# Kernel optimization log

Measured on AMD Instinct MI355X. Metric: run time of the kernel, lower is better.

Reference implementation:

```python
import jax, jax.numpy as jnp
import numpy as np

D = 256      # in_out_dimension
HID = 128    # hidden_dimension
N = 8192     # total nodes
S = 256      # number of graphs/segments


def setup_inputs() -> dict:
    key = jax.random.key(0)
    ks = jax.random.split(key, 20)
    lin = lambda k, o, i: jax.random.normal(k, (o, i), jnp.float32) * 0.05
    vec = lambda k, o: jax.random.normal(k, (o,), jnp.float32) * 0.05
    H = jax.random.normal(ks[0], (N, D), jnp.float32)
    batch = jnp.sort(jax.random.randint(ks[1], (N,), 0, S)).astype(jnp.int64)
    return {
        "H": H, "batch": batch,
        "phi_w1": lin(ks[2], D, D), "phi_b1": vec(ks[3], D),
        "phi_w2": lin(ks[4], D, D), "phi_b2": vec(ks[5], D),
        "att_w": lin(ks[6], D, D), "att_b": vec(ks[7], D),
        "rho_w1": lin(ks[8], D, D), "rho_b1": vec(ks[9], D),
        "rho_w2": lin(ks[10], D, D), "rho_b2": vec(ks[11], D),
        "g_w1": lin(ks[12], HID, D), "g_b1": vec(ks[13], HID),
        "g_w2": lin(ks[14], HID, HID), "g_b2": vec(ks[15], HID),
        "g_w3": lin(ks[16], 1, HID), "g_b3": vec(ks[17], 1),
    }


def _lrelu(x):
    return jax.nn.leaky_relu(x, negative_slope=0.01)


def reference(H, batch, phi_w1, phi_b1, phi_w2, phi_b2, att_w, att_b,
              rho_w1, rho_b1, rho_w2, rho_b2,
              g_w1, g_b1, g_w2, g_b2, g_w3, g_b3):
    # phi MLP
    Hf = _lrelu(_lrelu(H @ phi_w1.T + phi_b1) @ phi_w2.T + phi_b2)  # [N, D]
    att = Hf @ att_w.T + att_b                                      # [N, D]
    dot = att @ att.T                                               # [N, N]
    mask = (batch[:, None] == batch[None, :]).astype(Hf.dtype)      # block-diagonal
    # faithful to torch: max over (dot * mask), i.e. includes masked zeros
    max_values = jnp.max(dot * mask, axis=1, keepdims=True)         # [N, 1]
    mdp = (dot - max_values) * mask
    e = jnp.exp(mdp)
    aw = (e / jnp.sum(e * mask, axis=1, keepdims=True)) * mask      # [N, N]
    H_mixed = aw @ Hf                                               # [N, D]
    H_mixed = _lrelu(_lrelu(H_mixed @ rho_w1.T + rho_b1) @ rho_w2.T + rho_b2)
    h_gate = _lrelu(_lrelu(H_mixed @ g_w1.T + g_b1) @ g_w2.T + g_b2) @ g_w3.T + g_b3  # [N, 1]
    # scatter_softmax over segments
    seg_max = jax.ops.segment_max(h_gate, batch, num_segments=S)    # [S, 1]
    ex = jnp.exp(h_gate - seg_max[batch])
    den = jax.ops.segment_sum(ex, batch, num_segments=S)
    scores = ex / den[batch]                                        # [N, 1]
    h_pool = jax.ops.segment_sum(H_mixed * scores, batch, num_segments=S)  # [S, D]
    return (h_pool, scores)
```

## Files before the change

kernel.cpp:

```cpp
#include <hip/hip_runtime.h>
#include <math.h>

#define N_NODES 8192
#define D 256
#define HID 128
#define S_SEG 256
#define MAXC 64
#define HFT_STR 144
#define PB_STR 144
#define PB_LO 9216

typedef __attribute__((ext_vector_type(8))) short short8;
typedef __attribute__((ext_vector_type(4))) float f32x4;
typedef unsigned short u16;
typedef unsigned int u32;

__device__ __forceinline__ u16 f2bf(float f) {
  u32 u = __float_as_uint(f);
  u32 r = (u + 0x7fffu + ((u >> 16) & 1u)) >> 16;
  return (u16)r;
}
__device__ __forceinline__ float bf2f(u16 b) {
  return __uint_as_float(((u32)b) << 16);
}
__device__ __forceinline__ int4 pack8(float4 x, float4 y) {
  int4 v;
  v.x = (int)(((u32)f2bf(x.y) << 16) | f2bf(x.x));
  v.y = (int)(((u32)f2bf(x.w) << 16) | f2bf(x.z));
  v.z = (int)(((u32)f2bf(y.y) << 16) | f2bf(y.x));
  v.w = (int)(((u32)f2bf(y.w) << 16) | f2bf(y.z));
  return v;
}

struct CvtJobs {
  const float* src[7];
  u16* dst[7];
  int n4[7];
};
__global__ __launch_bounds__(256) void prep(const int* __restrict__ batch,
                                            int* __restrict__ sstart,
                                            int* __restrict__ scount, CvtJobs jb) {
  if (blockIdx.x == 0) {
    __shared__ int cntS[S_SEG];
    __shared__ int startS[S_SEG];
    const int t = threadIdx.x;
    cntS[t] = 0;
    startS[t] = 0;
    __syncthreads();
    const int base = t * 32;
    int pb = (base == 0) ? -1 : batch[base - 1];
    for (int i = 0; i < 32; ++i) {
      int b = batch[base + i];
      atomicAdd(&cntS[b], 1);
      if (b != pb) startS[b] = base + i;
      pb = b;
    }
    __syncthreads();
    scount[t] = cntS[t];
    sstart[t] = startS[t];
  } else {
    const int bid = blockIdx.x - 1;
    const int job = bid >> 3, chunk = bid & 7;
    const float* s = jb.src[job];
    u16* d = jb.dst[job];
    const int n4 = jb.n4[job];
    for (int i = chunk * 256 + threadIdx.x; i < n4; i += 2048) {
      float4 v = ((const float4*)s)[i];
      ushort4 o;
      o.x = f2bf(v.x); o.y = f2bf(v.y); o.z = f2bf(v.z); o.w = f2bf(v.w);
      ((ushort4*)d)[i] = o;
    }
  }
}

template <int KST>
__device__ __forceinline__ void loadW(short8* w, const u16* __restrict__ Wg,
                                      int col, int K, int lane) {
  const u16* base = Wg + (size_t)col * K + ((lane >> 4) * 8);
#pragma unroll
  for (int kk = 0; kk < KST; ++kk) w[kk] = *(const short8*)(base + kk * 32);
}

template <int KST, int ACT, int ISTR, int OSTR, int MODE, int MG>
__device__ __forceinline__ void mlp_phase(
    const u16* ldsIn, u16* ldsOut, u16* ldsOut2, const short8* wreg,
    const float* __restrict__ bias, int cg, int rows, int lane, int wave) {
  const int nrt = (rows + 31) >> 5;
  const int col = cg * 16 + (lane & 15);
  const float b = bias[col];
  int rt0, rt1;
  if constexpr (MG == 16) {
    rt0 = 0; rt1 = nrt;
  } else {
    rt0 = wave >> 3;
    rt1 = (rt0 < nrt) ? rt0 + 1 : rt0;
  }
  for (int rt = rt0; rt < rt1; ++rt) {
    short8 af[2][KST];
#pragma unroll
    for (int m = 0; m < 2; ++m)
#pragma unroll
      for (int kk = 0; kk < KST; ++kk) {
        const int r = rt * 32 + m * 16 + (lane & 15);
        const int sl = kk * 4 + (lane >> 4);
        af[m][kk] = *(const short8*)((const char*)ldsIn + r * ISTR +
                                     ((sl ^ (r & 7)) * 16));
      }
    f32x4 acc0 = {0.f, 0.f, 0.f, 0.f}, acc1 = {0.f, 0.f, 0.f, 0.f};
#pragma unroll
    for (int kk = 0; kk < KST; ++kk) {
      acc0 = __builtin_amdgcn_mfma_f32_16x16x32_bf16(af[0][kk], wreg[kk], acc0, 0, 0, 0);
      acc1 = __builtin_amdgcn_mfma_f32_16x16x32_bf16(af[1][kk], wreg[kk], acc1, 0, 0, 0);
    }
    const int rb = (lane >> 4) * 4;
#pragma unroll
    for (int m = 0; m < 2; ++m) {
      f32x4 a = m ? acc1 : acc0;
#pragma unroll
      for (int r4 = 0; r4 < 4; ++r4) {
        const int row = rt * 32 + m * 16 + rb + r4;
        if (row < rows) {
          float v = a[r4] + b;
          if (ACT) v = (v >= 0.f) ? v : 0.01f * v;
          if constexpr (MODE == 3) {
            const int byo =
                row * OSTR + (((col >> 3) ^ (row & 7)) * 16) + (col & 7) * 2;
            u16 hi = f2bf(v);
            *(u16*)((char*)ldsOut + byo) = hi;
            *(u16*)((char*)ldsOut2 + byo) = f2bf(v - bf2f(hi));
          } else if constexpr (MODE == 4) {
            u16 hv = f2bf(v);
            *(u16*)((char*)ldsOut + row * OSTR +
                    (((col >> 3) ^ (row & 7)) * 16) + (col & 7) * 2) = hv;
            *(u16*)((char*)ldsOut2 + col * HFT_STR + row * 2) = hv;
          } else {
            *(u16*)((char*)ldsOut + row * OSTR +
                    (((col >> 3) ^ (row & 7)) * 16) + (col & 7) * 2) = f2bf(v);
          }
        }
      }
    }
  }
}

template <int KST, int ACT, int ISTR, int OSTR, int MODE>
__device__ __forceinline__ void mlp16(
    const u16* ldsIn, u16* ldsOut, u16* ldsOut2, const u16* __restrict__ Wg,
    const float* __restrict__ bias, u16* __restrict__ gOut,
    u16* __restrict__ gOut2, int M, int K, int rows, int lane, int wave) {
  const int MG = M >> 4;
  const int npairs = ((rows + 31) >> 5) * MG;
  for (int p = wave; p < npairs; p += 16) {
    const int rt = p / MG, cg = p - rt * MG;
    short8 af[2][KST];
#pragma unroll
    for (int m = 0; m < 2; ++m)
#pragma unroll
      for (int kk = 0; kk < KST; ++kk) {
        const int r = rt * 32 + m * 16 + (lane & 15);
        const int sl = kk * 4 + (lane >> 4);
        af[m][kk] = *(const short8*)((const char*)ldsIn + r * ISTR +
                                     ((sl ^ (r & 7)) * 16));
      }
    const int col = cg * 16 + (lane & 15);
    short8 bfr[KST];
#pragma unroll
    for (int kk = 0; kk < KST; ++kk)
      bfr[kk] = *(const short8*)&Wg[(size_t)col * K + kk * 32 + (lane >> 4) * 8];
    f32x4 acc0 = {0.f, 0.f, 0.f, 0.f}, acc1 = {0.f, 0.f, 0.f, 0.f};
#pragma unroll
    for (int kk = 0; kk < KST; ++kk) {
      acc0 = __builtin_amdgcn_mfma_f32_16x16x32_bf16(af[0][kk], bfr[kk], acc0, 0, 0, 0);
      acc1 = __builtin_amdgcn_mfma_f32_16x16x32_bf16(af[1][kk], bfr[kk], acc1, 0, 0, 0);
    }
    const float b = bias[col];
    const int rb = (lane >> 4) * 4;
#pragma unroll
    for (int m = 0; m < 2; ++m) {
      f32x4 a = m ? acc1 : acc0;
#pragma unroll
      for (int r4 = 0; r4 < 4; ++r4) {
        const int row = rt * 32 + m * 16 + rb + r4;
        if (row < rows) {
          float v = a[r4] + b;
          if (ACT) v = (v >= 0.f) ? v : 0.01f * v;
          if constexpr (MODE == 2) {
            u16 hi = f2bf(v);
            gOut[(size_t)row * M + col] = hi;
            gOut2[(size_t)row * M + col] = f2bf(v - bf2f(hi));
          } else {
            u16 hv = f2bf(v);
            *(u16*)((char*)ldsOut + row * OSTR + (((col >> 3) ^ (row & 7)) * 16) +
                    (col & 7) * 2) = hv;
            if constexpr (MODE == 1) gOut[(size_t)row * M + col] = hv;
          }
        }
      }
    }
  }
}

__global__ __launch_bounds__(1024) void seg_all(
    const float* __restrict__ H, const u16* __restrict__ pw1,
    const float* __restrict__ pb1, const u16* __restrict__ pw2,
    const float* __restrict__ pb2, const u16* __restrict__ aw,
    const float* __restrict__ ab, const u16* __restrict__ rw1,
    const float* __restrict__ rb1, const u16* __restrict__ rw2,
    const float* __restrict__ rb2, const u16* __restrict__ gw1,
    const float* __restrict__ gb1, const u16* __restrict__ gw2,
    const float* __restrict__ gb2, const float* __restrict__ gw3,
    const float* __restrict__ gb3, const int* __restrict__ sstart,
    const int* __restrict__ scount, float* __restrict__ hpool,
    float* __restrict__ scores, u16* __restrict__ Hfg, u16* __restrict__ aHg,
    u16* __restrict__ aLg, u16* __restrict__ Hmg, u16* __restrict__ Hm2g,
    float* __restrict__ hgg) {
  __shared__ __align__(16) u16 bufX[MAXC * 256];
  __shared__ __align__(16) u16 bufY[MAXC * 256];
  __shared__ __align__(16) u16 attH[MAXC * 256];
  __shared__ __align__(16) u16 Tt[256 * 72];
  __shared__ float redP[64][4];
  __shared__ float hgs[MAXC];
  __shared__ float red[1024];
  __shared__ float part[1024];
  const int s = blockIdx.x, t = threadIdx.x;
  const int cnt = scount[s];
  const int r0 = sstart[s];
  const int wave = t >> 6, lane = t & 63;

  if (cnt == 0) {
    if (t < 256) hpool[(size_t)s * D + t] = 0.f;
    return;
  }

  if (cnt <= MAXC) {
    short8 wreg[8];
    const int cg16 = (wave + s) & 15;
    const int cg8 = ((wave & 7) + s) & 7;
    const int col16 = cg16 * 16 + (lane & 15);
    const int col8 = cg8 * 16 + (lane & 15);
    const int lrow = lane & 15;

    loadW<8>(wreg, pw1, col16, D, lane);
    {
      const int r = t >> 4, p16 = t & 15;
      if (r < cnt) {
        const float4* src = (const float4*)&H[(size_t)(r0 + r) * D + p16 * 16];
#pragma unroll
        for (int i = 0; i < 2; ++i) {
          int4 v = pack8(src[2 * i], src[2 * i + 1]);
          const int sl = p16 * 2 + i;
          *(int4*)((char*)bufX + r * 512 + ((sl ^ (r & 7)) * 16)) = v;
        }
      }
    }
    __syncthreads();
    mlp_phase<8, 1, 512, 512, 0, 16>(bufX, bufY, nullptr, wreg, pb1, cg16, cnt, lane, wave);
    loadW<8>(wreg, pw2, col16, D, lane);
    __syncthreads();
    mlp_phase<8, 1, 512, 512, 4, 16>(bufY, bufX, (u16*)Tt, wreg, pb2, cg16, cnt, lane, wave);
    loadW<8>(wreg, aw, col16, D, lane);
    __syncthreads();
    mlp_phase<8, 0, 512, 512, 3, 16>(bufX, attH, bufY, wreg, ab, cg16, cnt, lane, wave);
    __syncthreads();
    const int cp = (cnt + 15) & ~15;
    const int nt = cp >> 4;
    f32x4 ev = {0.f, 0.f, 0.f, 0.f};
    const int ttile = wave;
    const bool qact = ttile < nt * nt;
    int ti = 0, tj = 0;
    if (qact) {
      ti = ttile / nt; tj = ttile - ti * nt;
      const int ra = ti * 16 + lrow, rb2 = tj * 16 + lrow;
      f32x4 acc = {0.f, 0.f, 0.f, 0.f};
#pragma unroll
      for (int k0 = 0; k0 < D; k0 += 32) {
        const int sg = (k0 >> 3) + (lane >> 4);
        short8 ah = *(const short8*)((const char*)attH + ra * 512 + ((sg ^ (ra & 7)) * 16));
        short8 av = *(const short8*)((const char*)bufY + ra * 512 + ((sg ^ (ra & 7)) * 16));
        short8 bh = *(const short8*)((const char*)attH + rb2 * 512 + ((sg ^ (rb2 & 7)) * 16));
        short8 bv = *(const short8*)((const char*)bufY + rb2 * 512 + ((sg ^ (rb2 & 7)) * 16));
        acc = __builtin_amdgcn_mfma_f32_16x16x32_bf16(ah, bh, acc, 0, 0, 0);
        acc = __builtin_amdgcn_mfma_f32_16x16x32_bf16(ah, bv, acc, 0, 0, 0);
        acc = __builtin_amdgcn_mfma_f32_16x16x32_bf16(av, bh, acc, 0, 0, 0);
      }
      const int j = tj * 16 + lrow;
      const bool jok = j < cnt;
#pragma unroll
      for (int r = 0; r < 4; ++r) ev[r] = jok ? __expf(acc[r]) : 0.f;
      float p0 = ev[0], p1 = ev[1], p2 = ev[2], p3 = ev[3];
#pragma unroll
      for (int o = 1; o <= 8; o <<= 1) {
        p0 += __shfl_xor(p0, o); p1 += __shfl_xor(p1, o);
        p2 += __shfl_xor(p2, o); p3 += __shfl_xor(p3, o);
      }
      if ((lane & 15) == 0) {
        const int rbase = ti * 16 + (lane >> 4) * 4;
        redP[rbase + 0][tj] = p0;
        redP[rbase + 1][tj] = p1;
        redP[rbase + 2][tj] = p2;
        redP[rbase + 3][tj] = p3;
      }
    }
    __syncthreads();
    const int cpk = (cp <= 32) ? 32 : 64;
    if (qact) {
      const int j = tj * 16 + lrow;
      const int rbase = ti * 16 + (lane >> 4) * 4;
#pragma unroll
      for (int r = 0; r < 4; ++r) {
        float rs = 0.f;
        for (int q = 0; q < nt; ++q) rs += redP[rbase + r][q];
        const float pv = ev[r] / rs;
        const u16 hi = f2bf(pv);
        const u16 lo = f2bf(pv - bf2f(hi));
        *(u16*)((char*)bufY + (rbase + r) * PB_STR + j * 2) = hi;
        *(u16*)((char*)bufY + PB_LO + (rbase + r) * PB_STR + j * 2) = lo;
      }
    }
    if (cpk > cp) {
      const int w2 = cpk - cp;
      for (int idx = t; idx < cp * w2; idx += 1024) {
        const int rr = idx / w2, cc = cp + idx - (idx / w2) * w2;
        *(u16*)((char*)bufY + rr * PB_STR + cc * 2) = 0;
        *(u16*)((char*)bufY + PB_LO + rr * PB_STR + cc * 2) = 0;
      }
    }
    if (cpk > cnt) {
      const int w3 = cpk - cnt;
      for (int idx = t; idx < 256 * w3; idx += 1024) {
        const int dd = idx / w3, cc = cnt + idx - (idx / w3) * w3;
        *(u16*)((char*)Tt + dd * HFT_STR + cc * 2) = 0;
      }
    }
    __syncthreads();
    {
      const int kst = cpk >> 5;
      for (int tt = wave; tt < nt * 16; tt += 16) {
        const int rt = tt >> 4, cg = tt & 15;
        const int arow = rt * 16 + lrow;
        const int dcol = cg * 16 + lrow;
        const int koct = (lane >> 4) * 8;
        f32x4 acc = {0.f, 0.f, 0.f, 0.f};
        for (int ks = 0; ks < kst; ++ks) {
          const int kb = ks * 32 + koct;
          short8 ph = *(const short8*)((const char*)bufY + arow * PB_STR + kb * 2);
          short8 pl = *(const short8*)((const char*)bufY + PB_LO + arow * PB_STR + kb * 2);
          short8 hb = *(const short8*)((const char*)Tt + dcol * HFT_STR + kb * 2);
          acc = __builtin_amdgcn_mfma_f32_16x16x32_bf16(ph, hb, acc, 0, 0, 0);
          acc = __builtin_amdgcn_mfma_f32_16x16x32_bf16(pl, hb, acc, 0, 0, 0);
        }
        const int rb = (lane >> 4) * 4;
#pragma unroll
        for (int r = 0; r < 4; ++r) {
          const int row = rt * 16 + rb + r;
          const int col = cg * 16 + lrow;
          *(u16*)((char*)bufX + row * 512 + (((col >> 3) ^ (row & 7)) * 16) +
                  (col & 7) * 2) = f2bf(acc[r]);
        }
      }
    }
    loadW<8>(wreg, rw1, col16, D, lane);
    __syncthreads();
    mlp_phase<8, 1, 512, 512, 0, 16>(bufX, attH, nullptr, wreg, rb1, cg16, cnt, lane, wave);
    loadW<8>(wreg, rw2, col16, D, lane);
    __syncthreads();
    mlp_phase<8, 1, 512, 512, 0, 16>(attH, (u16*)Tt, nullptr, wreg, rb2, cg16, cnt, lane, wave);
    loadW<8>(wreg, gw1, col8, D, lane);
    __syncthreads();
    if (t < 64) hgs[t] = 0.f;
    mlp_phase<8, 1, 512, 256, 0, 8>((u16*)Tt, bufX, nullptr, wreg, gb1, cg8, cnt, lane, wave);
    loadW<4>(wreg, gw2, col8, HID, lane);
    __syncthreads();
    {
      const int nrt = (cnt + 31) >> 5;
      const int rt = wave >> 3;
      if (rt < nrt) {
        short8 af2[2][4];
#pragma unroll
        for (int m = 0; m < 2; ++m)
#pragma unroll
          for (int kk = 0; kk < 4; ++kk) {
            const int r = rt * 32 + m * 16 + (lane & 15);
            const int sl = kk * 4 + (lane >> 4);
            af2[m][kk] = *(const short8*)((const char*)bufX + r * 256 +
                                          ((sl ^ (r & 7)) * 16));
          }
        f32x4 acc0 = {0.f, 0.f, 0.f, 0.f}, acc1 = {0.f, 0.f, 0.f, 0.f};
#pragma unroll
        for (int kk = 0; kk < 4; ++kk) {
          acc0 = __builtin_amdgcn_mfma_f32_16x16x32_bf16(af2[0][kk], wreg[kk], acc0, 0, 0, 0);
          acc1 = __builtin_amdgcn_mfma_f32_16x16x32_bf16(af2[1][kk], wreg[kk], acc1, 0, 0, 0);
        }
        const float b = gb2[col8];
        const float w3c = gw3[col8];
        const int rb = (lane >> 4) * 4;
#pragma unroll
        for (int m = 0; m < 2; ++m) {
          f32x4 a = m ? acc1 : acc0;
#pragma unroll
          for (int r4 = 0; r4 < 4; ++r4) {
            const int row = rt * 32 + m * 16 + rb + r4;
            float v = a[r4] + b;
            v = (v >= 0.f) ? v : 0.01f * v;
            float pp = v * w3c;
            pp += __shfl_xor(pp, 1);
            pp += __shfl_xor(pp, 2);
            pp += __shfl_xor(pp, 4);
            pp += __shfl_xor(pp, 8);
            if ((lane & 15) == 0 && row < cnt) atomicAdd(&hgs[row], pp);
          }
        }
      }
    }
    __syncthreads();
    {
      const float hgv = (lane < cnt) ? hgs[lane] : -INFINITY;
      float m = hgv;
#pragma unroll
      for (int o = 32; o > 0; o >>= 1) m = fmaxf(m, __shfl_xor(m, o));
      float e = (lane < cnt) ? __expf(hgv - m) : 0.f;
      float sum = e;
#pragma unroll
      for (int o = 32; o > 0; o >>= 1) sum += __shfl_xor(sum, o);
      const float sc = e / sum;
      if (wave == 0 && lane < cnt) scores[r0 + lane] = sc;
      const int d = (wave & 3) * 64 + lane;
      const int g = wave >> 2;
      float acc = 0.f;
      for (int i = g; i < cnt; i += 4) {
        const float si = __shfl(sc, i);
        acc += si * bf2f(*(const u16*)((const char*)Tt + i * 512 +
                          (((d >> 3) ^ (i & 7)) * 16) + (d & 7) * 2));
      }
      part[g * 256 + d] = acc;
    }
    __syncthreads();
    if (t < 256)
      hpool[(size_t)s * D + t] =
          part[t] + part[t + 256] + part[t + 512] + part[t + 768];
  } else {
    for (int c0 = 0; c0 < cnt; c0 += 64) {
      const int rows = (cnt - c0) > 64 ? 64 : (cnt - c0);
      {
        const int r = t >> 4, p16 = t & 15;
        if (r < rows) {
          const float4* src = (const float4*)&H[(size_t)(r0 + c0 + r) * D + p16 * 16];
#pragma unroll
          for (int i = 0; i < 2; ++i) {
            int4 v = pack8(src[2 * i], src[2 * i + 1]);
            const int sl = p16 * 2 + i;
            *(int4*)((char*)bufX + r * 512 + ((sl ^ (r & 7)) * 16)) = v;
          }
        }
      }
      __syncthreads();
      mlp16<8, 1, 512, 512, 0>(bufX, bufY, nullptr, pw1, pb1, nullptr, nullptr, D, D, rows, lane, wave);
      __syncthreads();
      mlp16<8, 1, 512, 512, 1>(bufY, bufX, nullptr, pw2, pb2, Hfg + (size_t)(r0 + c0) * D, nullptr, D, D, rows, lane, wave);
      __syncthreads();
      mlp16<8, 0, 512, 512, 2>(bufX, nullptr, nullptr, aw, ab, aHg + (size_t)(r0 + c0) * D, aLg + (size_t)(r0 + c0) * D, D, D, rows, lane, wave);
      __syncthreads();
    }
    float* Pf = (float*)bufY;
    for (int i = 0; i < cnt; ++i) {
      const u16* ai = aHg + (size_t)(r0 + i) * D;
      const u16* li = aLg + (size_t)(r0 + i) * D;
      for (int j = t; j < cnt; j += 1024) {
        const u16* aj = aHg + (size_t)(r0 + j) * D;
        const u16* lj = aLg + (size_t)(r0 + j) * D;
        float acc = 0.f;
        for (int k = 0; k < D; ++k)
          acc += (bf2f(ai[k]) + bf2f(li[k])) * (bf2f(aj[k]) + bf2f(lj[k]));
        Pf[j] = acc;
      }
      __syncthreads();
      float pm = -INFINITY;
      for (int j = t; j < cnt; j += 1024) pm = fmaxf(pm, Pf[j]);
      red[t] = pm;
      __syncthreads();
      for (int o = 512; o > 0; o >>= 1) {
        if (t < o) red[t] = fmaxf(red[t], red[t + o]);
        __syncthreads();
      }
      const float m = red[0];
      __syncthreads();
      float ps = 0.f;
      for (int j = t; j < cnt; j += 1024) {
        const float e = __expf(Pf[j] - m);
        Pf[j] = e;
        ps += e;
      }
      red[t] = ps;
      __syncthreads();
      for (int o = 512; o > 0; o >>= 1) {
        if (t < o) red[t] += red[t + o];
        __syncthreads();
      }
      const float inv = 1.f / red[0];
      if (t < D) {
        float acc = 0.f;
        for (int j = 0; j < cnt; ++j)
          acc += Pf[j] * bf2f(Hfg[(size_t)(r0 + j) * D + t]);
        Hmg[(size_t)(r0 + i) * D + t] = f2bf(acc * inv);
      }
      __syncthreads();
    }
    for (int c0 = 0; c0 < cnt; c0 += 64) {
      const int rows = (cnt - c0) > 64 ? 64 : (cnt - c0);
      {
        const int r = t >> 4, p16 = t & 15;
        if (r < rows) {
          const int4* src = (const int4*)&Hmg[(size_t)(r0 + c0 + r) * D + p16 * 16];
#pragma unroll
          for (int i = 0; i < 2; ++i) {
            const int sl = p16 * 2 + i;
            *(int4*)((char*)bufX + r * 512 + ((sl ^ (r & 7)) * 16)) = src[i];
          }
        }
      }
      __syncthreads();
      mlp16<8, 1, 512, 512, 0>(bufX, bufY, nullptr, rw1, rb1, nullptr, nullptr, D, D, rows, lane, wave);
      __syncthreads();
      mlp16<8, 1, 512, 512, 1>(bufY, bufX, nullptr, rw2, rb2, Hm2g + (size_t)(r0 + c0) * D, nullptr, D, D, rows, lane, wave);
      __syncthreads();
      mlp16<8, 1, 512, 256, 0>(bufX, bufY, nullptr, gw1, gb1, nullptr, nullptr, HID, D, rows, lane, wave);
      __syncthreads();
      mlp16<4, 1, 256, 256, 0>(bufY, attH, nullptr, gw2, gb2, nullptr, nullptr, HID, HID, rows, lane, wave);
      __syncthreads();
      {
        const int i = t >> 4, p16 = t & 15;
        if (i < rows) {
          short8 hv = *(const short8*)((const char*)attH + i * 256 + ((p16 ^ (i & 7)) * 16));
          float sacc = 0.f;
#pragma unroll
          for (int q = 0; q < 8; ++q) sacc += bf2f((u16)hv[q]) * gw3[p16 * 8 + q];
          sacc += __shfl_xor(sacc, 1);
          sacc += __shfl_xor(sacc, 2);
          sacc += __shfl_xor(sacc, 4);
          sacc += __shfl_xor(sacc, 8);
          if (p16 == 0) hgg[r0 + c0 + i] = sacc + gb3[0];
        }
      }
      __syncthreads();
    }
    float pm = -INFINITY;
    for (int i = t; i < cnt; i += 1024) pm = fmaxf(pm, hgg[r0 + i]);
    red[t] = pm;
    __syncthreads();
    for (int o = 512; o > 0; o >>= 1) {
      if (t < o) red[t] = fmaxf(red[t], red[t + o]);
      __syncthreads();
    }
    const float m = red[0];
    __syncthreads();
    float ps = 0.f;
    for (int i = t; i < cnt; i += 1024) ps += __expf(hgg[r0 + i] - m);
    red[t] = ps;
    __syncthreads();
    for (int o = 512; o > 0; o >>= 1) {
      if (t < o) red[t] += red[t + o];
      __syncthreads();
    }
    const float inv = 1.f / red[0];
    for (int i = t; i < cnt; i += 1024)
      scores[r0 + i] = __expf(hgg[r0 + i] - m) * inv;
    const int h = t >> 8, d = t & 255;
    float acc = 0.f;
    for (int i = h; i < cnt; i += 4)
      acc += __expf(hgg[r0 + i] - m) * inv * bf2f(Hm2g[(size_t)(r0 + i) * D + d]);
    part[t] = acc;
    __syncthreads();
    if (t < 256)
      hpool[(size_t)s * D + t] =
          part[t] + part[t + 256] + part[t + 512] + part[t + 768];
  }
}

extern "C" void kernel_launch(void* const* d_in, const int* in_sizes, int n_in,
                              void* d_out, int out_size, void* d_ws, size_t ws_size,
                              hipStream_t stream) {
  const float* H      = (const float*)d_in[0];
  const int*   batch  = (const int*)d_in[1];
  const float* phi_w1 = (const float*)d_in[2];
  const float* phi_b1 = (const float*)d_in[3];
  const float* phi_w2 = (const float*)d_in[4];
  const float* phi_b2 = (const float*)d_in[5];
  const float* att_w  = (const float*)d_in[6];
  const float* att_b  = (const float*)d_in[7];
  const float* rho_w1 = (const float*)d_in[8];
  const float* rho_b1 = (const float*)d_in[9];
  const float* rho_w2 = (const float*)d_in[10];
  const float* rho_b2 = (const float*)d_in[11];
  const float* g_w1   = (const float*)d_in[12];
  const float* g_b1   = (const float*)d_in[13];
  const float* g_w2   = (const float*)d_in[14];
  const float* g_b2   = (const float*)d_in[15];
  const float* g_w3   = (const float*)d_in[16];
  const float* g_b3   = (const float*)d_in[17];

  float* out_hpool  = (float*)d_out;
  float* out_scores = (float*)d_out + (size_t)S_SEG * D;

  char* w = (char*)d_ws;
  const size_t MB = 1u << 20;
  u16*   wb     = (u16*)(w);
  u16*   Hfg    = (u16*)(w + 1 * MB);
  u16*   aHg    = (u16*)(w + 5 * MB);
  u16*   aLg    = (u16*)(w + 9 * MB);
  u16*   Hmg    = (u16*)(w + 13 * MB);
  u16*   Hm2g   = (u16*)(w + 17 * MB);
  float* hgg    = (float*)(w + 21 * MB);
  int*   sstart = (int*)(w + 21 * MB + 64 * 1024);
  int*   scount = sstart + S_SEG;

  u16* phi_w1b = wb;
  u16* phi_w2b = wb + 65536;
  u16* att_wb  = wb + 2 * 65536;
  u16* rho_w1b = wb + 3 * 65536;
  u16* rho_w2b = wb + 4 * 65536;
  u16* g_w1b   = wb + 5 * 65536;
  u16* g_w2b   = wb + 5 * 65536 + 32768;

  CvtJobs jb;
  jb.src[0] = phi_w1; jb.dst[0] = phi_w1b; jb.n4[0] = 65536 / 4;
  jb.src[1] = phi_w2; jb.dst[1] = phi_w2b; jb.n4[1] = 65536 / 4;
  jb.src[2] = att_w;  jb.dst[2] = att_wb;  jb.n4[2] = 65536 / 4;
  jb.src[3] = rho_w1; jb.dst[3] = rho_w1b; jb.n4[3] = 65536 / 4;
  jb.src[4] = rho_w2; jb.dst[4] = rho_w2b; jb.n4[4] = 65536 / 4;
  jb.src[5] = g_w1;   jb.dst[5] = g_w1b;   jb.n4[5] = 32768 / 4;
  jb.src[6] = g_w2;   jb.dst[6] = g_w2b;   jb.n4[6] = 16384 / 4;

  prep<<<57, 256, 0, stream>>>(batch, sstart, scount, jb);

  seg_all<<<S_SEG, 1024, 0, stream>>>(
      H, phi_w1b, phi_b1, phi_w2b, phi_b2, att_wb, att_b, rho_w1b, rho_b1,
      rho_w2b, rho_b2, g_w1b, g_b1, g_w2b, g_b2, g_w3, g_b3, sstart, scount,
      out_hpool, out_scores, Hfg, aHg, aLg, Hmg, Hm2g, hgg);
}
```

Before: 52.57 us.

## Split waves into row-tile by column-pair MLP work and fuse attention softmax per row

The per-segment MLP phases now assign each wave one 32-row tile and two 16-column groups (c and c+128). Previously each of 16 waves owned one column group and looped over every row tile. Weight loads for the next layer are double-buffered across the wA/wB register sets and issued around barriers. The attention dot/exp/row-sum step now gives each wave a whole 16-row strip, which removes the redP cross-wave reduction and one barrier. MFMA sections are wrapped in s_setprio and the LDS buffer roles are reshuffled. In exchange, waves beyond the needed row tiles sit idle when segments are small, and the doubled weight registers raise register pressure.

Result: slower. 75.38 us (+43.4%).

```diff
diff --git a/kernel.cpp b/kernel.cpp
--- a/kernel.cpp
+++ b/kernel.cpp
@@ -81,63 +81,105 @@
   for (int kk = 0; kk < KST; ++kk) w[kk] = *(const short8*)(base + kk * 32);
 }
 
-template <int KST, int ACT, int ISTR, int OSTR, int MODE, int MG>
-__device__ __forceinline__ void mlp_phase(
-    const u16* ldsIn, u16* ldsOut, u16* ldsOut2, const short8* wreg,
+template <int KST, int ACT, int OSTR, int MODE>
+__device__ __forceinline__ void mlp_pair(
+    const u16* ldsIn, u16* ldsOut, u16* ldsOut2, const short8* wA,
+    const short8* wB, const float* __restrict__ bias, int cg0, int rows,
+    int lane, int wave) {
+  const int rt = wave >> 3;
+  if (rt * 32 >= rows) return;
+  const int l15 = lane & 15;
+  const int c0 = cg0 * 16 + l15;
+  const int c1 = c0 + 128;
+  const float b0 = bias[c0], b1 = bias[c1];
+  const int rb = (lane >> 4) * 4;
+#pragma unroll
+  for (int m = 0; m < 2; ++m) {
+    short8 af[KST];
+#pragma unroll
+    for (int kk = 0; kk < KST; ++kk) {
+      const int r = rt * 32 + m * 16 + l15;
+      const int sl = kk * 4 + (lane >> 4);
+      af[kk] = *(const short8*)((const char*)ldsIn + r * 512 + ((sl ^ (r & 7)) * 16));
+    }
+    f32x4 a0 = {0.f, 0.f, 0.f, 0.f}, a1 = {0.f, 0.f, 0.f, 0.f};
+    __builtin_amdgcn_s_setprio(1);
+#pragma unroll
+    for (int kk = 0; kk < KST; ++kk)
+      a0 = __builtin_amdgcn_mfma_f32_16x16x32_bf16(af[kk], wA[kk], a0, 0, 0, 0);
+#pragma unroll
+    for (int kk = 0; kk < KST; ++kk)
+      a1 = __builtin_amdgcn_mfma_f32_16x16x32_bf16(af[kk], wB[kk], a1, 0, 0, 0);
+    __builtin_amdgcn_s_setprio(0);
+#pragma unroll
+    for (int r4 = 0; r4 < 4; ++r4) {
+      const int row = rt * 32 + m * 16 + rb + r4;
+      if (row < rows) {
+        float v0 = a0[r4] + b0, v1 = a1[r4] + b1;
+        if (ACT) {
+          v0 = (v0 >= 0.f) ? v0 : 0.01f * v0;
+          v1 = (v1 >= 0.f) ? v1 : 0.01f * v1;
+        }
+        if constexpr (MODE == 3) {
+          const int o0 = row * OSTR + (((c0 >> 3) ^ (row & 7)) * 16) + (c0 & 7) * 2;
+          const int o1 = row * OSTR + (((c1 >> 3) ^ (row & 7)) * 16) + (c1 & 7) * 2;
+          u16 h0 = f2bf(v0), h1 = f2bf(v1);
+          *(u16*)((char*)ldsOut + o0) = h0;
+          *(u16*)((char*)ldsOut2 + o0) = f2bf(v0 - bf2f(h0));
+          *(u16*)((char*)ldsOut + o1) = h1;
+          *(u16*)((char*)ldsOut2 + o1) = f2bf(v1 - bf2f(h1));
+        } else if constexpr (MODE == 4) {
+          u16 h0 = f2bf(v0), h1 = f2bf(v1);
+          *(u16*)((char*)ldsOut + row * OSTR + (((c0 >> 3) ^ (row & 7)) * 16) +
+                  (c0 & 7) * 2) = h0;
+          *(u16*)((char*)ldsOut + row * OSTR + (((c1 >> 3) ^ (row & 7)) * 16) +
+                  (c1 & 7) * 2) = h1;
+          *(u16*)((char*)ldsOut2 + c0 * HFT_STR + row * 2) = h0;
+          *(u16*)((char*)ldsOut2 + c1 * HFT_STR + row * 2) = h1;
+        } else {
+          *(u16*)((char*)ldsOut + row * OSTR + (((c0 >> 3) ^ (row & 7)) * 16) +
+                  (c0 & 7) * 2) = f2bf(v0);
+          *(u16*)((char*)ldsOut + row * OSTR + (((c1 >> 3) ^ (row & 7)) * 16) +
+                  (c1 & 7) * 2) = f2bf(v1);
+        }
+      }
+    }
+  }
+}
+
+template <int KST, int ACT, int ISTR, int OSTR>
+__device__ __forceinline__ void mlp_g(
+    const u16* ldsIn, u16* ldsOut, const short8* wreg,
     const float* __restrict__ bias, int cg, int rows, int lane, int wave) {
   const int nrt = (rows + 31) >> 5;
+  const int rt = wave >> 3;
+  if (rt >= nrt) return;
   const int col = cg * 16 + (lane & 15);
   const float b = bias[col];
-  int rt0, rt1;
-  if constexpr (MG == 16) {
-    rt0 = 0; rt1 = nrt;
-  } else {
-    rt0 = wave >> 3;
-    rt1 = (rt0 < nrt) ? rt0 + 1 : rt0;
-  }
-  for (int rt = rt0; rt < rt1; ++rt) {
-    short8 af[2][KST];
-#pragma unroll
-    for (int m = 0; m < 2; ++m)
-#pragma unroll
-      for (int kk = 0; kk < KST; ++kk) {
-        const int r = rt * 32 + m * 16 + (lane & 15);
-        const int sl = kk * 4 + (lane >> 4);
-        af[m][kk] = *(const short8*)((const char*)ldsIn + r * ISTR +
-                                     ((sl ^ (r & 7)) * 16));
-      }
-    f32x4 acc0 = {0.f, 0.f, 0.f, 0.f}, acc1 = {0.f, 0.f, 0.f, 0.f};
+  short8 af[KST];
+#pragma unroll
+  for (int m = 0; m < 2; ++m) {
 #pragma unroll
     for (int kk = 0; kk < KST; ++kk) {
-      acc0 = __builtin_amdgcn_mfma_f32_16x16x32_bf16(af[0][kk], wreg[kk], acc0, 0, 0, 0);
-      acc1 = __builtin_amdgcn_mfma_f32_16x16x32_bf16(af[1][kk], wreg[kk], acc1, 0, 0, 0);
-    }
+      const int r = rt * 32 + m * 16 + (lane & 15);
+      const int sl = kk * 4 + (lane >> 4);
+      af[kk] = *(const short8*)((const char*)ldsIn + r * ISTR + ((sl ^ (r & 7)) * 16));
+    }
+    f32x4 acc = {0.f, 0.f, 0.f, 0.f};
+    __builtin_amdgcn_s_setprio(1);
+#pragma unroll
+    for (int kk = 0; kk < KST; ++kk)
+      acc = __builtin_amdgcn_mfma_f32_16x16x32_bf16(af[kk], wreg[kk], acc, 0, 0, 0);
+    __builtin_amdgcn_s_setprio(0);
     const int rb = (lane >> 4) * 4;
 #pragma unroll
-    for (int m = 0; m < 2; ++m) {
-      f32x4 a = m ? acc1 : acc0;
-#pragma unroll
-      for (int r4 = 0; r4 < 4; ++r4) {
-        const int row = rt * 32 + m * 16 + rb + r4;
-        if (row < rows) {
-          float v = a[r4] + b;
-          if (ACT) v = (v >= 0.f) ? v : 0.01f * v;
-          if constexpr (MODE == 3) {
-            const int byo =
-                row * OSTR + (((col >> 3) ^ (row & 7)) * 16) + (col & 7) * 2;
-            u16 hi = f2bf(v);
-            *(u16*)((char*)ldsOut + byo) = hi;
-            *(u16*)((char*)ldsOut2 + byo) = f2bf(v - bf2f(hi));
-          } else if constexpr (MODE == 4) {
-            u16 hv = f2bf(v);
-            *(u16*)((char*)ldsOut + row * OSTR +
-                    (((col >> 3) ^ (row & 7)) * 16) + (col & 7) * 2) = hv;
-            *(u16*)((char*)ldsOut2 + col * HFT_STR + row * 2) = hv;
-          } else {
-            *(u16*)((char*)ldsOut + row * OSTR +
-                    (((col >> 3) ^ (row & 7)) * 16) + (col & 7) * 2) = f2bf(v);
-          }
-        }
+    for (int r4 = 0; r4 < 4; ++r4) {
+      const int row = rt * 32 + m * 16 + rb + r4;
+      if (row < rows) {
+        float v = acc[r4] + b;
+        if (ACT) v = (v >= 0.f) ? v : 0.01f * v;
+        *(u16*)((char*)ldsOut + row * OSTR + (((col >> 3) ^ (row & 7)) * 16) +
+                (col & 7) * 2) = f2bf(v);
       }
     }
   }
@@ -218,7 +260,6 @@
   __shared__ __align__(16) u16 bufY[MAXC * 256];
   __shared__ __align__(16) u16 attH[MAXC * 256];
   __shared__ __align__(16) u16 Tt[256 * 72];
-  __shared__ float redP[64][4];
   __shared__ float hgs[MAXC];
   __shared__ float red[1024];
   __shared__ float part[1024];
@@ -233,14 +274,14 @@
   }
 
   if (cnt <= MAXC) {
-    short8 wreg[8];
-    const int cg16 = (wave + s) & 15;
-    const int cg8 = ((wave & 7) + s) & 7;
-    const int col16 = cg16 * 16 + (lane & 15);
-    const int col8 = cg8 * 16 + (lane & 15);
-    const int lrow = lane & 15;
-
-    loadW<8>(wreg, pw1, col16, D, lane);
+    short8 wA[8], wB[8];
+    const int cg0 = ((wave & 7) + s) & 7;
+    const int colA = cg0 * 16 + (lane & 15);
+    const int colB = colA + 128;
+    const int l15 = lane & 15;
+
+    loadW<8>(wA, pw1, colA, D, lane);
+    loadW<8>(wB, pw1, colB, D, lane);
     {
       const int r = t >> 4, p16 = t & 15;
       if (r < cnt) {
@@ -254,75 +295,78 @@
       }
     }
     __syncthreads();
-    mlp_phase<8, 1, 512, 512, 0, 16>(bufX, bufY, nullptr, wreg, pb1, cg16, cnt, lane, wave);
-    loadW<8>(wreg, pw2, col16, D, lane);
-    __syncthreads();
-    mlp_phase<8, 1, 512, 512, 4, 16>(bufY, bufX, (u16*)Tt, wreg, pb2, cg16, cnt, lane, wave);
-    loadW<8>(wreg, aw, col16, D, lane);
-    __syncthreads();
-    mlp_phase<8, 0, 512, 512, 3, 16>(bufX, attH, bufY, wreg, ab, cg16, cnt, lane, wave);
+    mlp_pair<8, 1, 512, 0>(bufX, bufY, nullptr, wA, wB, pb1, cg0, cnt, lane, wave);
+    loadW<8>(wA, pw2, colA, D, lane);
+    __syncthreads();
+    loadW<8>(wB, pw2, colB, D, lane);
+    mlp_pair<8, 1, 512, 4>(bufY, bufX, (u16*)Tt, wA, wB, pb2, cg0, cnt, lane, wave);
+    loadW<8>(wA, aw, colA, D, lane);
+    __syncthreads();
+    loadW<8>(wB, aw, colB, D, lane);
+    mlp_pair<8, 0, 512, 3>(bufX, attH, bufY, wA, wB, ab, cg0, cnt, lane, wave);
+    loadW<8>(wA, rw1, colA, D, lane);
     __syncthreads();
     const int cp = (cnt + 15) & ~15;
     const int nt = cp >> 4;
-    f32x4 ev = {0.f, 0.f, 0.f, 0.f};
-    const int ttile = wave;
-    const bool qact = ttile < nt * nt;
-    int ti = 0, tj = 0;
-    if (qact) {
-      ti = ttile / nt; tj = ttile - ti * nt;
-      const int ra = ti * 16 + lrow, rb2 = tj * 16 + lrow;
-      f32x4 acc = {0.f, 0.f, 0.f, 0.f};
-#pragma unroll
-      for (int k0 = 0; k0 < D; k0 += 32) {
-        const int sg = (k0 >> 3) + (lane >> 4);
-        short8 ah = *(const short8*)((const char*)attH + ra * 512 + ((sg ^ (ra & 7)) * 16));
-        short8 av = *(const short8*)((const char*)bufY + ra * 512 + ((sg ^ (ra & 7)) * 16));
-        short8 bh = *(const short8*)((const char*)attH + rb2 * 512 + ((sg ^ (rb2 & 7)) * 16));
-        short8 bv = *(const short8*)((const char*)bufY + rb2 * 512 + ((sg ^ (rb2 & 7)) * 16));
-        acc = __builtin_amdgcn_mfma_f32_16x16x32_bf16(ah, bh, acc, 0, 0, 0);
-        acc = __builtin_amdgcn_mfma_f32_16x16x32_bf16(ah, bv, acc, 0, 0, 0);
-        acc = __builtin_amdgcn_mfma_f32_16x16x32_bf16(av, bh, acc, 0, 0, 0);
-      }
-      const int j = tj * 16 + lrow;
-      const bool jok = j < cnt;
-#pragma unroll
-      for (int r = 0; r < 4; ++r) ev[r] = jok ? __expf(acc[r]) : 0.f;
-      float p0 = ev[0], p1 = ev[1], p2 = ev[2], p3 = ev[3];
-#pragma unroll
-      for (int o = 1; o <= 8; o <<= 1) {
-        p0 += __shfl_xor(p0, o); p1 += __shfl_xor(p1, o);
-        p2 += __shfl_xor(p2, o); p3 += __shfl_xor(p3, o);
-      }
-      if ((lane & 15) == 0) {
-        const int rbase = ti * 16 + (lane >> 4) * 4;
-        redP[rbase + 0][tj] = p0;
-        redP[rbase + 1][tj] = p1;
-        redP[rbase + 2][tj] = p2;
-        redP[rbase + 3][tj] = p3;
-      }
-    }
-    __syncthreads();
     const int cpk = (cp <= 32) ? 32 : 64;
-    if (qact) {
-      const int j = tj * 16 + lrow;
+    if (wave < nt) {
+      const int ti = wave;
+      const int ra = ti * 16 + l15;
+      f32x4 evt[4];
+      f32x4 rs = {0.f, 0.f, 0.f, 0.f};
+#pragma unroll
+      for (int tj = 0; tj < 4; ++tj) {
+        if (tj < nt) {
+          const int rj = tj * 16 + l15;
+          f32x4 acc = {0.f, 0.f, 0.f, 0.f};
+          __builtin_amdgcn_s_setprio(1);
+#pragma unroll
+          for (int k0 = 0; k0 < D; k0 += 32) {
+            const int sg = (k0 >> 3) + (lane >> 4);
+            short8 ah = *(const short8*)((const char*)attH + ra * 512 + ((sg ^ (ra & 7)) * 16));
+            short8 av = *(const short8*)((const char*)bufY + ra * 512 + ((sg ^ (ra & 7)) * 16));
+            short8 bh = *(const short8*)((const char*)attH + rj * 512 + ((sg ^ (rj & 7)) * 16));
+            short8 bv = *(const short8*)((const char*)bufY + rj * 512 + ((sg ^ (rj & 7)) * 16));
+            acc = __builtin_amdgcn_mfma_f32_16x16x32_bf16(ah, bh, acc, 0, 0, 0);
+            acc = __builtin_amdgcn_mfma_f32_16x16x32_bf16(ah, bv, acc, 0, 0, 0);
+            acc = __builtin_amdgcn_mfma_f32_16x16x32_bf16(av, bh, acc, 0, 0, 0);
+          }
+          __builtin_amdgcn_s_setprio(0);
+          const bool jok = (tj * 16 + l15) < cnt;
+          f32x4 ev;
+#pragma unroll
+          for (int r = 0; r < 4; ++r) ev[r] = jok ? __expf(acc[r]) : 0.f;
+          evt[tj] = ev;
+          float p0 = ev[0], p1 = ev[1], p2 = ev[2], p3 = ev[3];
+#pragma unroll
+          for (int o = 1; o <= 8; o <<= 1) {
+            p0 += __shfl_xor(p0, o); p1 += __shfl_xor(p1, o);
+            p2 += __shfl_xor(p2, o); p3 += __shfl_xor(p3, o);
+          }
+          rs[0] += p0; rs[1] += p1; rs[2] += p2; rs[3] += p3;
+        }
+      }
       const int rbase = ti * 16 + (lane >> 4) * 4;
 #pragma unroll
-      for (int r = 0; r < 4; ++r) {
-        float rs = 0.f;
-        for (int q = 0; q < nt; ++q) rs += redP[rbase + r][q];
-        const float pv = ev[r] / rs;
-        const u16 hi = f2bf(pv);
-        const u16 lo = f2bf(pv - bf2f(hi));
-        *(u16*)((char*)bufY + (rbase + r) * PB_STR + j * 2) = hi;
-        *(u16*)((char*)bufY + PB_LO + (rbase + r) * PB_STR + j * 2) = lo;
+      for (int tj = 0; tj < 4; ++tj) {
+        if (tj < nt) {
+          const int j = tj * 16 + l15;
+#pragma unroll
+          for (int r = 0; r < 4; ++r) {
+            const float pv = evt[tj][r] / rs[r];
+            const u16 hi = f2bf(pv);
+            *(u16*)((char*)bufX + (rbase + r) * PB_STR + j * 2) = hi;
+            *(u16*)((char*)bufX + PB_LO + (rbase + r) * PB_STR + j * 2) =
+                f2bf(pv - bf2f(hi));
+          }
+        }
       }
     }
     if (cpk > cp) {
-      const int w2 = cpk - cp;
-      for (int idx = t; idx < cp * w2; idx += 1024) {
-        const int rr = idx / w2, cc = cp + idx - (idx / w2) * w2;
-        *(u16*)((char*)bufY + rr * PB_STR + cc * 2) = 0;
-        *(u16*)((char*)bufY + PB_LO + rr * PB_STR + cc * 2) = 0;
+      for (int idx = t; idx < cp * 16; idx += 1024) {
+        const int rr = idx >> 4, cc = cp + (idx & 15);
+        *(u16*)((char*)bufX + rr * PB_STR + cc * 2) = 0;
+        *(u16*)((char*)bufX + PB_LO + rr * PB_STR + cc * 2) = 0;
       }
     }
     if (cpk > cnt) {
@@ -337,60 +381,72 @@
       const int kst = cpk >> 5;
       for (int tt = wave; tt < nt * 16; tt += 16) {
         const int rt = tt >> 4, cg = tt & 15;
-        const int arow = rt * 16 + lrow;
-        const int dcol = cg * 16 + lrow;
+        const int arow = rt * 16 + l15;
+        const int dcol = cg * 16 + l15;
         const int koct = (lane >> 4) * 8;
         f32x4 acc = {0.f, 0.f, 0.f, 0.f};
+        __builtin_amdgcn_s_setprio(1);
         for (int ks = 0; ks < kst; ++ks) {
           const int kb = ks * 32 + koct;
-          short8 ph = *(const short8*)((const char*)bufY + arow * PB_STR + kb * 2);
-          short8 pl = *(const short8*)((const char*)bufY + PB_LO + arow * PB_STR + kb * 2);
+          short8 ph = *(const short8*)((const char*)bufX + arow * PB_STR + kb * 2);
+          short8 pl = *(const short8*)((const char*)bufX + PB_LO + arow * PB_STR + kb * 2);
           short8 hb = *(const short8*)((const char*)Tt + dcol * HFT_STR + kb * 2);
           acc = __builtin_amdgcn_mfma_f32_16x16x32_bf16(ph, hb, acc, 0, 0, 0);
           acc = __builtin_amdgcn_mfma_f32_16x16x32_bf16(pl, hb, acc, 0, 0, 0);
         }
+        __builtin_amdgcn_s_setprio(0);
         const int rb = (lane >> 4) * 4;
 #pragma unroll
         for (int r = 0; r < 4; ++r) {
           const int row = rt * 16 + rb + r;
-          const int col = cg * 16 + lrow;
-          *(u16*)((char*)bufX + row * 512 + (((col >> 3) ^ (row & 7)) * 16) +
+          const int col = cg * 16 + l15;
+          *(u16*)((char*)attH + row * 512 + (((col >> 3) ^ (row & 7)) * 16) +
                   (col & 7) * 2) = f2bf(acc[r]);
         }
       }
     }
-    loadW<8>(wreg, rw1, col16, D, lane);
-    __syncthreads();
-    mlp_phase<8, 1, 512, 512, 0, 16>(bufX, attH, nullptr, wreg, rb1, cg16, cnt, lane, wave);
-    loadW<8>(wreg, rw2, col16, D, lane);
-    __syncthreads();
-    mlp_phase<8, 1, 512, 512, 0, 16>(attH, (u16*)Tt, nullptr, wreg, rb2, cg16, cnt, lane, wave);
-    loadW<8>(wreg, gw1, col8, D, lane);
+    __syncthreads();
+    loadW<8>(wB, rw1, colB, D, lane);
+    mlp_pair<8, 1, 512, 0>(attH, bufY, nullptr, wA, wB, rb1, cg0, cnt, lane, wave);
+    loadW<8>(wA, rw2, colA, D, lane);
+    __syncthreads();
+    loadW<8>(wB, rw2, colB, D, lane);
+    mlp_pair<8, 1, 512, 0>(bufY, (u16*)Tt, nullptr, wA, wB, rb2, cg0, cnt, lane, wave);
+    loadW<8>(wA, gw1, ((cg0)*16 + l15), D, lane);
     __syncthreads();
     if (t < 64) hgs[t] = 0.f;
-    mlp_phase<8, 1, 512, 256, 0, 8>((u16*)Tt, bufX, nullptr, wreg, gb1, cg8, cnt, lane, wave);
-    loadW<4>(wreg, gw2, col8, HID, lane);
+    mlp_g<8, 1, 512, 256>((u16*)Tt, bufX, wA, gb1, cg0, cnt, lane, wave);
+    loadW<4>(wB, gw2, ((cg0)*16 + l15), HID, lane);
     __syncthreads();
     {
       const int nrt = (cnt + 31) >> 5;
       const int rt = wave >> 3;
+      const int col8 = cg0 * 16 + l15;
       if (rt < nrt) {
-        short8 af2[2][4];
-#pragma unroll
-        for (int m = 0; m < 2; ++m)
-#pragma unroll
-          for (int kk = 0; kk < 4; ++kk) {
-            const int r = rt * 32 + m * 16 + (lane & 15);
-            const int sl = kk * 4 + (lane >> 4);
-            af2[m][kk] = *(const short8*)((const char*)bufX + r * 256 +
-                                          ((sl ^ (r & 7)) * 16));
-          }
         f32x4 acc0 = {0.f, 0.f, 0.f, 0.f}, acc1 = {0.f, 0.f, 0.f, 0.f};
+        short8 af2[4];
 #pragma unroll
         for (int kk = 0; kk < 4; ++kk) {
-          acc0 = __builtin_amdgcn_mfma_f32_16x16x32_bf16(af2[0][kk], wreg[kk], acc0, 0, 0, 0);
-          acc1 = __builtin_amdgcn_mfma_f32_16x16x32_bf16(af2[1][kk], wreg[kk], acc1, 0, 0, 0);
-        }
+          const int r = rt * 32 + l15;
+          const int sl = kk * 4 + (lane >> 4);
+          af2[kk] = *(const short8*)((const char*)bufX + r * 256 + ((sl ^ (r & 7)) * 16));
+        }
+        __builtin_amdgcn_s_setprio(1);
+#pragma unroll
+        for (int kk = 0; kk < 4; ++kk)
+          acc0 = __builtin_amdgcn_mfma_f32_16x16x32_bf16(af2[kk], wB[kk], acc0, 0, 0, 0);
+        __builtin_amdgcn_s_setprio(0);
+#pragma unroll
+        for (int kk = 0; kk < 4; ++kk) {
+          const int r = rt * 32 + 16 + l15;
+          const int sl = kk * 4 + (lane >> 4);
+          af2[kk] = *(const short8*)((const char*)bufX + r * 256 + ((sl ^ (r & 7)) * 16));
+        }
+        __builtin_amdgcn_s_setprio(1);
+#pragma unroll
+        for (int kk = 0; kk < 4; ++kk)
+          acc1 = __builtin_amdgcn_mfma_f32_16x16x32_bf16(af2[kk], wB[kk], acc1, 0, 0, 0);
+        __builtin_amdgcn_s_setprio(0);
         const float b = gb2[col8];
         const float w3c = gw3[col8];
         const int rb = (lane >> 4) * 4;
```

## Compute full attention row per wave, drop redP barrier, add MFMA priority hints

Applied to the files above, without the earlier changes.

The attention-score stage now has each wave own one 16-row tile and loop over all column tiles. Row sums are accumulated in registers, which removes the redP shared array and one block-wide barrier. Buffers are reassigned (probabilities in bufX, mixed output in attH, rho1 output in bufY) so the rw1 weight load can be issued before the barrier and overlap the attention work. s_setprio hints wrap the MFMA loops. Fewer waves now do the score work (nt instead of nt*nt), so the serial chain inside each wave gets longer.

After: 53.28 us. Within noise of the previous version (+1.3%).

```diff
diff --git a/kernel.cpp b/kernel.cpp
--- a/kernel.cpp
+++ b/kernel.cpp
@@ -107,11 +107,13 @@
                                      ((sl ^ (r & 7)) * 16));
       }
     f32x4 acc0 = {0.f, 0.f, 0.f, 0.f}, acc1 = {0.f, 0.f, 0.f, 0.f};
+    __builtin_amdgcn_s_setprio(1);
 #pragma unroll
     for (int kk = 0; kk < KST; ++kk) {
       acc0 = __builtin_amdgcn_mfma_f32_16x16x32_bf16(af[0][kk], wreg[kk], acc0, 0, 0, 0);
       acc1 = __builtin_amdgcn_mfma_f32_16x16x32_bf16(af[1][kk], wreg[kk], acc1, 0, 0, 0);
     }
+    __builtin_amdgcn_s_setprio(0);
     const int rb = (lane >> 4) * 4;
 #pragma unroll
     for (int m = 0; m < 2; ++m) {
@@ -218,7 +220,6 @@
   __shared__ __align__(16) u16 bufY[MAXC * 256];
   __shared__ __align__(16) u16 attH[MAXC * 256];
   __shared__ __align__(16) u16 Tt[256 * 72];
-  __shared__ float redP[64][4];
   __shared__ float hgs[MAXC];
   __shared__ float red[1024];
   __shared__ float part[1024];
@@ -238,7 +239,7 @@
     const int cg8 = ((wave & 7) + s) & 7;
     const int col16 = cg16 * 16 + (lane & 15);
     const int col8 = cg8 * 16 + (lane & 15);
-    const int lrow = lane & 15;
+    const int l15 = lane & 15;
 
     loadW<8>(wreg, pw1, col16, D, lane);
     {
@@ -261,68 +262,69 @@
     loadW<8>(wreg, aw, col16, D, lane);
     __syncthreads();
     mlp_phase<8, 0, 512, 512, 3, 16>(bufX, attH, bufY, wreg, ab, cg16, cnt, lane, wave);
+    loadW<8>(wreg, rw1, col16, D, lane);
     __syncthreads();
     const int cp = (cnt + 15) & ~15;
     const int nt = cp >> 4;
-    f32x4 ev = {0.f, 0.f, 0.f, 0.f};
-    const int ttile = wave;
-    const bool qact = ttile < nt * nt;
-    int ti = 0, tj = 0;
-    if (qact) {
-      ti = ttile / nt; tj = ttile - ti * nt;
-      const int ra = ti * 16 + lrow, rb2 = tj * 16 + lrow;
-      f32x4 acc = {0.f, 0.f, 0.f, 0.f};
-#pragma unroll
-      for (int k0 = 0; k0 < D; k0 += 32) {
-        const int sg = (k0 >> 3) + (lane >> 4);
-        short8 ah = *(const short8*)((const char*)attH + ra * 512 + ((sg ^ (ra & 7)) * 16));
-        short8 av = *(const short8*)((const char*)bufY + ra * 512 + ((sg ^ (ra & 7)) * 16));
-        short8 bh = *(const short8*)((const char*)attH + rb2 * 512 + ((sg ^ (rb2 & 7)) * 16));
-        short8 bv = *(const short8*)((const char*)bufY + rb2 * 512 + ((sg ^ (rb2 & 7)) * 16));
-        acc = __builtin_amdgcn_mfma_f32_16x16x32_bf16(ah, bh, acc, 0, 0, 0);
-        acc = __builtin_amdgcn_mfma_f32_16x16x32_bf16(ah, bv, acc, 0, 0, 0);
-        acc = __builtin_amdgcn_mfma_f32_16x16x32_bf16(av, bh, acc, 0, 0, 0);
-      }
-      const int j = tj * 16 + lrow;
-      const bool jok = j < cnt;
-#pragma unroll
-      for (int r = 0; r < 4; ++r) ev[r] = jok ? __expf(acc[r]) : 0.f;
-      float p0 = ev[0], p1 = ev[1], p2 = ev[2], p3 = ev[3];
-#pragma unroll
-      for (int o = 1; o <= 8; o <<= 1) {
-        p0 += __shfl_xor(p0, o); p1 += __shfl_xor(p1, o);
-        p2 += __shfl_xor(p2, o); p3 += __shfl_xor(p3, o);
-      }
-      if ((lane & 15) == 0) {
-        const int rbase = ti * 16 + (lane >> 4) * 4;
-        redP[rbase + 0][tj] = p0;
-        redP[rbase + 1][tj] = p1;
-        redP[rbase + 2][tj] = p2;
-        redP[rbase + 3][tj] = p3;
-      }
-    }
-    __syncthreads();
     const int cpk = (cp <= 32) ? 32 : 64;
-    if (qact) {
-      const int j = tj * 16 + lrow;
+    if (wave < nt) {
+      const int ti = wave;
+      const int ra = ti * 16 + l15;
+      f32x4 evt[4];
+      f32x4 rs = {0.f, 0.f, 0.f, 0.f};
+#pragma unroll
+      for (int tj = 0; tj < 4; ++tj) {
+        if (tj < nt) {
+          const int rj = tj * 16 + l15;
+          f32x4 acc = {0.f, 0.f, 0.f, 0.f};
+          __builtin_amdgcn_s_setprio(1);
+#pragma unroll
+          for (int k0 = 0; k0 < D; k0 += 32) {
+            const int sg = (k0 >> 3) + (lane >> 4);
+            short8 ah = *(const short8*)((const char*)attH + ra * 512 + ((sg ^ (ra & 7)) * 16));
+            short8 av = *(const short8*)((const char*)bufY + ra * 512 + ((sg ^ (ra & 7)) * 16));
+            short8 bh = *(const short8*)((const char*)attH + rj * 512 + ((sg ^ (rj & 7)) * 16));
+            short8 bv = *(const short8*)((const char*)bufY + rj * 512 + ((sg ^ (rj & 7)) * 16));
+            acc = __builtin_amdgcn_mfma_f32_16x16x32_bf16(ah, bh, acc, 0, 0, 0);
+            acc = __builtin_amdgcn_mfma_f32_16x16x32_bf16(ah, bv, acc, 0, 0, 0);
+            acc = __builtin_amdgcn_mfma_f32_16x16x32_bf16(av, bh, acc, 0, 0, 0);
+          }
+          __builtin_amdgcn_s_setprio(0);
+          const bool jok = (tj * 16 + l15) < cnt;
+          f32x4 ev;
+#pragma unroll
+          for (int r = 0; r < 4; ++r) ev[r] = jok ? __expf(acc[r]) : 0.f;
+          evt[tj] = ev;
+          float p0 = ev[0], p1 = ev[1], p2 = ev[2], p3 = ev[3];
+#pragma unroll
+          for (int o = 1; o <= 8; o <<= 1) {
+            p0 += __shfl_xor(p0, o); p1 += __shfl_xor(p1, o);
+            p2 += __shfl_xor(p2, o); p3 += __shfl_xor(p3, o);
+          }
+          rs[0] += p0; rs[1] += p1; rs[2] += p2; rs[3] += p3;
+        }
+      }
       const int rbase = ti * 16 + (lane >> 4) * 4;
 #pragma unroll
-      for (int r = 0; r < 4; ++r) {
-        float rs = 0.f;
-        for (int q = 0; q < nt; ++q) rs += redP[rbase + r][q];
-        const float pv = ev[r] / rs;
-        const u16 hi = f2bf(pv);
-        const u16 lo = f2bf(pv - bf2f(hi));
-        *(u16*)((char*)bufY + (rbase + r) * PB_STR + j * 2) = hi;
-        *(u16*)((char*)bufY + PB_LO + (rbase + r) * PB_STR + j * 2) = lo;
+      for (int tj = 0; tj < 4; ++tj) {
+        if (tj < nt) {
+          const int j = tj * 16 + l15;
+#pragma unroll
+          for (int r = 0; r < 4; ++r) {
+            const float pv = evt[tj][r] / rs[r];
+            const u16 hi = f2bf(pv);
+            *(u16*)((char*)bufX + (rbase + r) * PB_STR + j * 2) = hi;
+            *(u16*)((char*)bufX + PB_LO + (rbase + r) * PB_STR + j * 2) =
+                f2bf(pv - bf2f(hi));
+          }
+        }
       }
     }
     if (cpk > cp) {
-      const int w2 = cpk - cp;
-      for (int idx = t; idx < cp * w2; idx += 1024) {
-        const int rr = idx / w2, cc = cp + idx - (idx / w2) * w2;
-        *(u16*)((char*)bufY + rr * PB_STR + cc * 2) = 0;
-        *(u16*)((char*)bufY + PB_LO + rr * PB_STR + cc * 2) = 0;
+      for (int idx = t; idx < cp * 16; idx += 1024) {
+        const int rr = idx >> 4, cc = cp + (idx & 15);
+        *(u16*)((char*)bufX + rr * PB_STR + cc * 2) = 0;
+        *(u16*)((char*)bufX + PB_LO + rr * PB_STR + cc * 2) = 0;
       }
     }
     if (cpk > cnt) {
@@ -337,34 +339,35 @@
       const int kst = cpk >> 5;
       for (int tt = wave; tt < nt * 16; tt += 16) {
         const int rt = tt >> 4, cg = tt & 15;
-        const int arow = rt * 16 + lrow;
-        const int dcol = cg * 16 + lrow;
+        const int arow = rt * 16 + l15;
+        const int dcol = cg * 16 + l15;
         const int koct = (lane >> 4) * 8;
         f32x4 acc = {0.f, 0.f, 0.f, 0.f};
+        __builtin_amdgcn_s_setprio(1);
         for (int ks = 0; ks < kst; ++ks) {
           const int kb = ks * 32 + koct;
-          short8 ph = *(const short8*)((const char*)bufY + arow * PB_STR + kb * 2);
-          short8 pl = *(const short8*)((const char*)bufY + PB_LO + arow * PB_STR + kb * 2);
+          short8 ph = *(const short8*)((const char*)bufX + arow * PB_STR + kb * 2);
+          short8 pl = *(const short8*)((const char*)bufX + PB_LO + arow * PB_STR + kb * 2);
           short8 hb = *(const short8*)((const char*)Tt + dcol * HFT_STR + kb * 2);
           acc = __builtin_amdgcn_mfma_f32_16x16x32_bf16(ph, hb, acc, 0, 0, 0);
           acc = __builtin_amdgcn_mfma_f32_16x16x32_bf16(pl, hb, acc, 0, 0, 0);
         }
+        __builtin_amdgcn_s_setprio(0);
         const int rb = (lane >> 4) * 4;
 #pragma unroll
         for (int r = 0; r < 4; ++r) {
           const int row = rt * 16 + rb + r;
-          const int col = cg * 16 + lrow;
-          *(u16*)((char*)bufX + row * 512 + (((col >> 3) ^ (row & 7)) * 16) +
+          const int col = cg * 16 + l15;
+          *(u16*)((char*)attH + row * 512 + (((col >> 3) ^ (row & 7)) * 16) +
                   (col & 7) * 2) = f2bf(acc[r]);
         }
       }
     }
-    loadW<8>(wreg, rw1, col16, D, lane);
-    __syncthreads();
-    mlp_phase<8, 1, 512, 512, 0, 16>(bufX, attH, nullptr, wreg, rb1, cg16, cnt, lane, wave);
+    __syncthreads();
+    mlp_phase<8, 1, 512, 512, 0, 16>(attH, bufY, nullptr, wreg, rb1, cg16, cnt, lane, wave);
     loadW<8>(wreg, rw2, col16, D, lane);
     __syncthreads();
-    mlp_phase<8, 1, 512, 512, 0, 16>(attH, (u16*)Tt, nullptr, wreg, rb2, cg16, cnt, lane, wave);
+    mlp_phase<8, 1, 512, 512, 0, 16>(bufY, (u16*)Tt, nullptr, wreg, rb2, cg16, cnt, lane, wave);
     loadW<8>(wreg, gw1, col8, D, lane);
     __syncthreads();
     if (t < 64) hgs[t] = 0.f;
@@ -380,17 +383,19 @@
         for (int m = 0; m < 2; ++m)
 #pragma unroll
           for (int kk = 0; kk < 4; ++kk) {
-            const int r = rt * 32 + m * 16 + (lane & 15);
+            const int r = rt * 32 + m * 16 + l15;
             const int sl = kk * 4 + (lane >> 4);
             af2[m][kk] = *(const short8*)((const char*)bufX + r * 256 +
                                           ((sl ^ (r & 7)) * 16));
           }
         f32x4 acc0 = {0.f, 0.f, 0.f, 0.f}, acc1 = {0.f, 0.f, 0.f, 0.f};
+        __builtin_amdgcn_s_setprio(1);
 #pragma unroll
         for (int kk = 0; kk < 4; ++kk) {
           acc0 = __builtin_amdgcn_mfma_f32_16x16x32_bf16(af2[0][kk], wreg[kk], acc0, 0, 0, 0);
           acc1 = __builtin_amdgcn_mfma_f32_16x16x32_bf16(af2[1][kk], wreg[kk], acc1, 0, 0, 0);
         }
+        __builtin_amdgcn_s_setprio(0);
         const float b = gb2[col8];
         const float w3c = gw3[col8];
         const int rb = (lane >> 4) * 4;
```
